# Performance work log

Hardware: AMD Instinct MI355X
Metric: run time of the kernel (lower is better)

## Reference

```python
import jax, jax.numpy as jnp
import numpy as np

EMBED_DIM = 2048
NUM_HEADS = 32
NUM_KV_HEADS = 8
HEAD_DIM = EMBED_DIM // NUM_HEADS  # 64
KV_DIM = HEAD_DIM * NUM_KV_HEADS   # 512
Q_PER_KV = NUM_HEADS // NUM_KV_HEADS  # 4


def setup_inputs() -> dict:
    key = jax.random.key(0)
    ks = jax.random.split(key, 9)
    s = 1.0 / np.sqrt(EMBED_DIM)
    x = jax.random.normal(ks[0], (2, 2048, EMBED_DIM), dtype=jnp.float32)
    Wq = jax.random.uniform(ks[1], (EMBED_DIM, EMBED_DIM), jnp.float32, -s, s)
    bq = jax.random.uniform(ks[2], (EMBED_DIM,), jnp.float32, -s, s)
    Wk = jax.random.uniform(ks[3], (KV_DIM, EMBED_DIM), jnp.float32, -s, s)
    bk = jax.random.uniform(ks[4], (KV_DIM,), jnp.float32, -s, s)
    Wv = jax.random.uniform(ks[5], (KV_DIM, EMBED_DIM), jnp.float32, -s, s)
    bv = jax.random.uniform(ks[6], (KV_DIM,), jnp.float32, -s, s)
    Wo = jax.random.uniform(ks[7], (EMBED_DIM, EMBED_DIM), jnp.float32, -s, s)
    bo = jax.random.uniform(ks[8], (EMBED_DIM,), jnp.float32, -s, s)
    return {"x": x, "Wq": Wq, "bq": bq, "Wk": Wk, "bk": bk,
            "Wv": Wv, "bv": bv, "Wo": Wo, "bo": bo}


def reference(x, Wq, bq, Wk, bk, Wv, bv, Wo, bo):
    B, S, E = x.shape
    # projections (torch Linear: x @ W.T + b)
    q = x @ Wq.T + bq                       # [B,S,E]
    k = x @ Wk.T + bk                       # [B,S,KV_DIM]
    v = x @ Wv.T + bv
    # [B, num_kv, q_per_kv, S, D] and [B, num_kv, S, D] -- GQA grouping
    # avoids repeat_interleave duplication while computing identical math
    q = q.reshape(B, S, NUM_KV_HEADS, Q_PER_KV, HEAD_DIM).transpose(0, 2, 3, 1, 4)
    k = k.reshape(B, S, NUM_KV_HEADS, HEAD_DIM).transpose(0, 2, 1, 3)
    v = v.reshape(B, S, NUM_KV_HEADS, HEAD_DIM).transpose(0, 2, 1, 3)
    scale = 1.0 / np.sqrt(HEAD_DIM).astype(np.float32)
    scores = jnp.einsum('bgqsd,bgtd->bgqst', q, k) * scale  # [B,G,Qpk,S,S]
    causal = jnp.triu(jnp.ones((S, S), dtype=bool), k=1)
    scores = jnp.where(causal, jnp.float32(-jnp.inf), scores)
    attn = jax.nn.softmax(scores, axis=-1)
    out = jnp.einsum('bgqst,bgtd->bgqsd', attn, v)          # [B,G,Qpk,S,D]
    # back to [B,S,E]: head order matches repeat_interleave (kv-major)
    out = out.transpose(0, 3, 1, 2, 4).reshape(B, S, E)
    return out @ Wo.T + bo
```

## Files before the change

kernel.cpp:

```cpp
#include <hip/hip_runtime.h>
#include <stdint.h>

#define EMBED  2048
#define SEQ    2048
#define BATCH  2
#define NHEADS 32
#define NKV    8
#define HDIM   64
#define KVD    512
#define MTOT   (BATCH*SEQ)
#define QKVN   (EMBED + 2*KVD)

typedef __bf16 bf16x8 __attribute__((ext_vector_type(8)));
typedef float  f32x4  __attribute__((ext_vector_type(4)));
typedef float  f32x8v __attribute__((ext_vector_type(8)));
typedef float  f32x2v __attribute__((ext_vector_type(2)));
typedef float  f32x16 __attribute__((ext_vector_type(16)));

#define QSCALE 0.18033688f
#define M2     11.541560f

static __device__ __forceinline__ unsigned short f2bf(float f) {
    union { float f; unsigned int u; } v; v.f = f;
    return (unsigned short)((v.u + 0x7fffu + ((v.u >> 16) & 1u)) >> 16);
}

static __device__ __forceinline__ void gload_lds16(const void* g, void* l) {
    __builtin_amdgcn_global_load_lds(
        (const __attribute__((address_space(1))) void*)g,
        (__attribute__((address_space(3))) void*)l, 16, 0, 0);
}

template<int N> static __device__ __forceinline__ void waitvm() {
    if constexpr (N == 2) asm volatile("s_waitcnt vmcnt(2)" ::: "memory");
    else if constexpr (N == 3) asm volatile("s_waitcnt vmcnt(3)" ::: "memory");
    else if constexpr (N == 5) asm volatile("s_waitcnt vmcnt(5)" ::: "memory");
    else asm volatile("s_waitcnt vmcnt(4)" ::: "memory");
}

static __device__ __forceinline__ void cast4(const float* __restrict__ in,
                                             unsigned short* __restrict__ out, int i) {
    float4 f = reinterpret_cast<const float4*>(in)[i];
    ushort4 o;
    o.x = f2bf(f.x); o.y = f2bf(f.y); o.z = f2bf(f.z); o.w = f2bf(f.w);
    reinterpret_cast<ushort4*>(out)[i] = o;
}

__global__ __launch_bounds__(256)
void prep(const float* __restrict__ x,  const float* __restrict__ Wq,
          const float* __restrict__ Wk, const float* __restrict__ Wv,
          const float* __restrict__ Wo, const float* __restrict__ bq,
          const float* __restrict__ bk, const float* __restrict__ bv,
          unsigned short* __restrict__ xb, unsigned short* __restrict__ Wqkvb,
          unsigned short* __restrict__ Wob, float* __restrict__ bqkv)
{
    const int t0 = blockIdx.x * blockDim.x + threadIdx.x;
    const int st = gridDim.x * blockDim.x;
    for (int i = t0; i < (MTOT * EMBED) / 4;  i += st) cast4(x,  xb, i);
    for (int i = t0; i < (EMBED * EMBED) / 4; i += st) cast4(Wq, Wqkvb, i);
    for (int i = t0; i < (KVD * EMBED) / 4;   i += st) cast4(Wk, Wqkvb + EMBED * EMBED, i);
    for (int i = t0; i < (KVD * EMBED) / 4;   i += st) cast4(Wv, Wqkvb + (EMBED + KVD) * EMBED, i);
    for (int i = t0; i < (EMBED * EMBED) / 4; i += st) cast4(Wo, Wob, i);
    if (t0 < QKVN / 4) {
        float4 v = (t0 < EMBED / 4) ? reinterpret_cast<const float4*>(bq)[t0]
                 : (t0 < (EMBED + KVD) / 4) ? reinterpret_cast<const float4*>(bk)[t0 - EMBED / 4]
                 : reinterpret_cast<const float4*>(bv)[t0 - (EMBED + KVD) / 4];
        reinterpret_cast<float4*>(bqkv)[t0] = v;
    }
}

__global__ __launch_bounds__(256)
void transpose_v(const unsigned short* __restrict__ qkv,
                 unsigned short* __restrict__ vt)
{
    __shared__ __align__(16) unsigned short T[64][72];
    const int bg = blockIdx.x & 15;
    const int bt = blockIdx.x >> 4;
    const int b  = bg >> 3, g = bg & 7;
    const int tid = threadIdx.x;
    const int tr  = tid >> 2, c = tid & 3;

    const unsigned short* src = qkv + ((size_t)(b * SEQ + bt * 64 + tr)) * QKVN
                              + (EMBED + KVD) + g * HDIM + c * 16;
    uint4 v0 = *reinterpret_cast<const uint4*>(src);
    uint4 v1 = *reinterpret_cast<const uint4*>(src + 8);
    *reinterpret_cast<uint4*>(&T[tr][c * 16])     = v0;
    *reinterpret_cast<uint4*>(&T[tr][c * 16 + 8]) = v1;
    __syncthreads();

    const int dr = tr;
    unsigned short o[16];
#pragma unroll
    for (int j = 0; j < 16; ++j) o[j] = T[c * 16 + j][dr];
    unsigned short* dst = vt + ((size_t)(bg * 64 + dr)) * SEQ + bt * 64 + c * 16;
    *reinterpret_cast<uint4*>(dst)     = *reinterpret_cast<uint4*>(o);
    *reinterpret_cast<uint4*>(dst + 8) = *reinterpret_cast<uint4*>(o + 8);
}

__global__ __launch_bounds__(512, 1)
void gemm192(const unsigned short* __restrict__ A,
             const unsigned short* __restrict__ B,
             const float* __restrict__ bias,
             unsigned short* __restrict__ C, int M, int N, int K)
{
    constexpr int ASZ   = 256 * 128;
    constexpr int BSZ   = 192 * 128;
    constexpr int AHALF = ASZ / 2;
    constexpr int BUFSZ = ASZ + BSZ;

    __shared__ __align__(16) char lds[2 * BUFSZ];

    const int tid = threadIdx.x;
    const int l   = tid & 63;
    const int w   = tid >> 6;
    const int wr  = w >> 2, wc = w & 3;
    const int lr15 = l & 15;
    const int lkb  = (l >> 4) * 16;

    const int nwg = gridDim.x;
    const int cpx = nwg >> 3;
    const int bid = blockIdx.x;
    const int swz = (bid & 7) * cpx + (bid >> 3);
    const int NMB = M / 256;
    const int m0  = (swz % NMB) * 256;
    const int n0  = (swz / NMB) * 192;

    unsigned offA[2][2], dA[2][2];
#pragma unroll
    for (int q = 0; q < 2; ++q)
#pragma unroll
        for (int j = 0; j < 2; ++j) {
            int L  = q * AHALF + (tid + j * 512) * 16;
            int R  = L >> 7;
            int cb = (L & 127) ^ ((R & 7) << 4);
            int lrow = ((R >> 6) & 1) * 128 + (R >> 7) * 64 + (R & 63);
            offA[q][j] = (unsigned)((m0 + lrow) * K * 2 + cb);
            dA[q][j]   = (unsigned)L;
        }
    unsigned offB[3], dB[3];
#pragma unroll
    for (int q = 0; q < 3; ++q) {
        int L  = q * 8192 + tid * 16;
        int R  = L >> 7;
        int cb = (L & 127) ^ ((R & 7) << 4);
        offB[q] = (unsigned)((n0 + R) * K * 2 + cb);
        dB[q]   = (unsigned)(ASZ + L);
    }

#define STAGE_A(q, bw, ku) { _Pragma("unroll") \
    for (int j_ = 0; j_ < 2; ++j_) \
        gload_lds16((const char*)A + offA[q][j_] + (unsigned)(ku) * 128u, (bw) + dA[q][j_]); }
#define STAGE_B(q, bw, ku) \
    gload_lds16((const char*)B + offB[q] + (unsigned)(ku) * 128u, (bw) + dB[q]);

    auto rdA = [&](const char* br, int mi, int kk) -> bf16x8 {
        int row  = (mi >> 2) * 128 + wr * 64 + (mi & 3) * 16 + lr15;
        int byte = (row * 128 + kk * 64 + lkb) ^ ((row & 7) << 4);
        return *reinterpret_cast<const bf16x8*>(br + byte);
    };
    auto rdB = [&](const char* br, int ni, int kk) -> bf16x8 {
        int row  = ni * 64 + wc * 16 + lr15;
        int byte = (row * 128 + kk * 64 + lkb) ^ ((row & 7) << 4);
        return *reinterpret_cast<const bf16x8*>(br + ASZ + byte);
    };

    f32x4 acc[8][3] = {};
    bf16x8 afrLo[4][2], afrHi[4][2], bf[3][2];

    STAGE_A(0, lds, 0); STAGE_B(0, lds, 0); STAGE_B(1, lds, 0);
    STAGE_B(2, lds, 0); STAGE_A(1, lds, 0);
    waitvm<3>();
    __builtin_amdgcn_s_barrier();
#pragma unroll
    for (int mi = 0; mi < 4; ++mi)
#pragma unroll
        for (int kk = 0; kk < 2; ++kk) afrLo[mi][kk] = rdA(lds, mi, kk);
#pragma unroll
    for (int kk = 0; kk < 2; ++kk) bf[0][kk] = rdB(lds, 0, kk);

    const int NKT = K >> 6;
    for (int u = 0; u < NKT; ++u) {
        char* br = lds + (u & 1) * BUFSZ;
        char* bw = lds + ((u & 1) ^ 1) * BUFSZ;
        const bool pf = (u + 1 < NKT);
        const int  ku = u + 1;

        if (pf) STAGE_A(0, bw, ku);
#pragma unroll
        for (int kk = 0; kk < 2; ++kk) bf[1][kk] = rdB(br, 1, kk);
        __builtin_amdgcn_s_setprio(1);
#pragma unroll
        for (int mi = 0; mi < 4; ++mi)
#pragma unroll
            for (int kk = 0; kk < 2; ++kk)
                acc[mi][0] = __builtin_amdgcn_mfma_f32_16x16x32_bf16(afrLo[mi][kk], bf[0][kk], acc[mi][0], 0, 0, 0);
        __builtin_amdgcn_s_setprio(0);
        waitvm<4>();
        __builtin_amdgcn_s_barrier();

        if (pf) STAGE_B(0, bw, ku);
#pragma unroll
        for (int kk = 0; kk < 2; ++kk) bf[2][kk] = rdB(br, 2, kk);
        __builtin_amdgcn_s_setprio(1);
#pragma unroll
        for (int mi = 0; mi < 4; ++mi)
#pragma unroll
            for (int kk = 0; kk < 2; ++kk)
                acc[mi][1] = __builtin_amdgcn_mfma_f32_16x16x32_bf16(afrLo[mi][kk], bf[1][kk], acc[mi][1], 0, 0, 0);
        __builtin_amdgcn_s_setprio(0);
        waitvm<3>();
        __builtin_amdgcn_s_barrier();

        if (pf) STAGE_B(1, bw, ku);
#pragma unroll
        for (int mi = 0; mi < 4; ++mi)
#pragma unroll
            for (int kk = 0; kk < 2; ++kk) afrHi[mi][kk] = rdA(br, 4 + mi, kk);
        __builtin_amdgcn_s_setprio(1);
#pragma unroll
        for (int mi = 0; mi < 4; ++mi)
#pragma unroll
            for (int kk = 0; kk < 2; ++kk)
                acc[mi][2] = __builtin_amdgcn_mfma_f32_16x16x32_bf16(afrLo[mi][kk], bf[2][kk], acc[mi][2], 0, 0, 0);
        __builtin_amdgcn_s_setprio(0);

        if (pf) STAGE_B(2, bw, ku);
        __builtin_amdgcn_s_setprio(1);
#pragma unroll
        for (int mi = 0; mi < 4; ++mi)
#pragma unroll
            for (int kk = 0; kk < 2; ++kk)
                acc[4 + mi][0] = __builtin_amdgcn_mfma_f32_16x16x32_bf16(afrHi[mi][kk], bf[0][kk], acc[4 + mi][0], 0, 0, 0);
        __builtin_amdgcn_s_setprio(0);

        if (pf) STAGE_A(1, bw, ku);
        __builtin_amdgcn_s_setprio(1);
#pragma unroll
        for (int mi = 0; mi < 4; ++mi)
#pragma unroll
            for (int kk = 0; kk < 2; ++kk)
                acc[4 + mi][1] = __builtin_amdgcn_mfma_f32_16x16x32_bf16(afrHi[mi][kk], bf[1][kk], acc[4 + mi][1], 0, 0, 0);
        __builtin_amdgcn_s_setprio(0);

        __builtin_amdgcn_s_setprio(1);
#pragma unroll
        for (int mi = 0; mi < 4; ++mi)
#pragma unroll
            for (int kk = 0; kk < 2; ++kk)
                acc[4 + mi][2] = __builtin_amdgcn_mfma_f32_16x16x32_bf16(afrHi[mi][kk], bf[2][kk], acc[4 + mi][2], 0, 0, 0);
        __builtin_amdgcn_s_setprio(0);
        waitvm<3>();
        __builtin_amdgcn_s_barrier();
        if (pf) {
#pragma unroll
            for (int mi = 0; mi < 4; ++mi)
#pragma unroll
                for (int kk = 0; kk < 2; ++kk) afrLo[mi][kk] = rdA(bw, mi, kk);
#pragma unroll
            for (int kk = 0; kk < 2; ++kk) bf[0][kk] = rdB(bw, 0, kk);
        }
    }
#undef STAGE_A
#undef STAGE_B

    float bv[3];
#pragma unroll
    for (int ni = 0; ni < 3; ++ni) bv[ni] = bias[n0 + ni * 64 + wc * 16 + lr15];
#pragma unroll
    for (int mi = 0; mi < 8; ++mi)
#pragma unroll
        for (int ni = 0; ni < 3; ++ni)
#pragma unroll
            for (int r = 0; r < 4; ++r) {
                int row = m0 + wr * 128 + mi * 16 + (l >> 4) * 4 + r;
                int col = n0 + ni * 64 + wc * 16 + lr15;
                C[(size_t)row * N + col] = f2bf(acc[mi][ni][r] + bv[ni]);
            }
}

template<int WM, bool OUT_BF16>
__global__ __launch_bounds__(512, 1)
void gemm8p(const unsigned short* __restrict__ A,
            const unsigned short* __restrict__ B,
            const float* __restrict__ bias,
            void* __restrict__ C, int M, int N, int K)
{
    constexpr int BM    = WM * 32;
    constexpr int ASZ   = BM * 128;
    constexpr int BSZ   = 256 * 128;
    constexpr int AHALF = ASZ / 2;
    constexpr int AL    = AHALF / 8192;
    constexpr int BUFSZ = ASZ + BSZ;

    __shared__ __align__(16) char lds[2 * BUFSZ];

    const int tid = threadIdx.x;
    const int l   = tid & 63;
    const int w   = tid >> 6;
    const int wr  = w >> 2, wc = w & 3;
    const int lr15 = l & 15;
    const int lkb  = (l >> 4) * 16;

    const int nwg = gridDim.x;
    const int cpx = nwg >> 3;
    const int bid = blockIdx.x;
    const int swz = (bid & 7) * cpx + (bid >> 3);
    const int NMB = M / BM;
    const int m0  = (swz % NMB) * BM;
    const int n0  = (swz / NMB) * 256;

    unsigned offA[2][AL], dA[2][AL];
#pragma unroll
    for (int q = 0; q < 2; ++q)
#pragma unroll
        for (int j = 0; j < AL; ++j) {
            int L  = q * AHALF + (tid + j * 512) * 16;
            int R  = L >> 7;
            int cb = (L & 127) ^ ((R & 7) << 4);
            int lrow;
            if constexpr (WM == 8) lrow = ((R >> 6) & 1) * 128 + (R >> 7) * 64 + (R & 63);
            else                   lrow = ((R >> 5) & 1) * 64  + (R >> 6) * 32 + (R & 31);
            offA[q][j] = (unsigned)((m0 + lrow) * K * 2 + cb);
            dA[q][j]   = (unsigned)L;
        }
    unsigned offB[2][2], dB[2][2];
#pragma unroll
    for (int q = 0; q < 2; ++q)
#pragma unroll
        for (int j = 0; j < 2; ++j) {
            int L  = q * 16384 + (tid + j * 512) * 16;
            int R  = L >> 7;
            int cb = (L & 127) ^ ((R & 7) << 4);
            int lrow = ((R >> 5) & 3) * 64 + (R >> 7) * 32 + (R & 31);
            offB[q][j] = (unsigned)((n0 + lrow) * K * 2 + cb);
            dB[q][j]   = (unsigned)(ASZ + L);
        }

#define STAGE_A(q, bw, ku) { _Pragma("unroll") \
    for (int j_ = 0; j_ < AL; ++j_) \
        gload_lds16((const char*)A + offA[q][j_] + (unsigned)(ku) * 128u, (bw) + dA[q][j_]); }
#define STAGE_B(q, bw, ku) { _Pragma("unroll") \
    for (int j_ = 0; j_ < 2; ++j_) \
        gload_lds16((const char*)B + offB[q][j_] + (unsigned)(ku) * 128u, (bw) + dB[q][j_]); }

    auto rdA = [&](const char* br, int mi, int kk) -> bf16x8 {
        int row;
        if constexpr (WM == 8) row = (mi >> 2) * 128 + wr * 64 + (mi & 3) * 16 + lr15;
        else                   row = (mi >> 1) * 64  + wr * 32 + (mi & 1) * 16 + lr15;
        int byte = (row * 128 + kk * 64 + lkb) ^ ((row & 7) << 4);
        return *reinterpret_cast<const bf16x8*>(br + byte);
    };
    auto rdB = [&](const char* br, int ni, int kk) -> bf16x8 {
        int row  = (ni >> 1) * 128 + wc * 32 + (ni & 1) * 16 + lr15;
        int byte = (row * 128 + kk * 64 + lkb) ^ ((row & 7) << 4);
        return *reinterpret_cast<const bf16x8*>(br + ASZ + byte);
    };

    f32x4 acc[WM][4] = {};
    bf16x8 afr[WM / 2][2], bf0[2][2], bf1[2][2];

    STAGE_A(0, lds, 0); STAGE_B(0, lds, 0); STAGE_B(1, lds, 0); STAGE_A(1, lds, 0);
    waitvm<2 + AL>();
    __builtin_amdgcn_s_barrier();

    const int NKT = K >> 6;
    for (int u = 0; u < NKT; ++u) {
        char* br = lds + (u & 1) * BUFSZ;
        char* bw = lds + ((u & 1) ^ 1) * BUFSZ;
        const bool pf = (u + 1 < NKT);
        const int  ku = u + 1;

        if (pf) STAGE_A(0, bw, ku);
#pragma unroll
        for (int mi = 0; mi < WM / 2; ++mi)
#pragma unroll
            for (int kk = 0; kk < 2; ++kk) afr[mi][kk] = rdA(br, mi, kk);
#pragma unroll
        for (int ni = 0; ni < 2; ++ni)
#pragma unroll
            for (int kk = 0; kk < 2; ++kk) bf0[ni][kk] = rdB(br, ni, kk);
        __builtin_amdgcn_s_setprio(1);
#pragma unroll
        for (int mi = 0; mi < WM / 2; ++mi)
#pragma unroll
            for (int ni = 0; ni < 2; ++ni)
#pragma unroll
                for (int kk = 0; kk < 2; ++kk)
                    acc[mi][ni] = __builtin_amdgcn_mfma_f32_16x16x32_bf16(afr[mi][kk], bf0[ni][kk], acc[mi][ni], 0, 0, 0);
        __builtin_amdgcn_s_setprio(0);
        waitvm<2 * AL>();
        __builtin_amdgcn_s_barrier();

        if (pf) STAGE_B(0, bw, ku);
#pragma unroll
        for (int ni = 0; ni < 2; ++ni)
#pragma unroll
            for (int kk = 0; kk < 2; ++kk) bf1[ni][kk] = rdB(br, 2 + ni, kk);
        __builtin_amdgcn_s_setprio(1);
#pragma unroll
        for (int mi = 0; mi < WM / 2; ++mi)
#pragma unroll
            for (int ni = 0; ni < 2; ++ni)
#pragma unroll
                for (int kk = 0; kk < 2; ++kk)
                    acc[mi][2 + ni] = __builtin_amdgcn_mfma_f32_16x16x32_bf16(afr[mi][kk], bf1[ni][kk], acc[mi][2 + ni], 0, 0, 0);
        __builtin_amdgcn_s_setprio(0);
        waitvm<AL + 2>();
        __builtin_amdgcn_s_barrier();

        if (pf) STAGE_B(1, bw, ku);
#pragma unroll
        for (int mi = 0; mi < WM / 2; ++mi)
#pragma unroll
            for (int kk = 0; kk < 2; ++kk) afr[mi][kk] = rdA(br, WM / 2 + mi, kk);
        __builtin_amdgcn_s_setprio(1);
#pragma unroll
        for (int mi = 0; mi < WM / 2; ++mi)
#pragma unroll
            for (int ni = 0; ni < 2; ++ni)
#pragma unroll
                for (int kk = 0; kk < 2; ++kk)
                    acc[WM / 2 + mi][ni] = __builtin_amdgcn_mfma_f32_16x16x32_bf16(afr[mi][kk], bf0[ni][kk], acc[WM / 2 + mi][ni], 0, 0, 0);
        __builtin_amdgcn_s_setprio(0);

        if (pf) STAGE_A(1, bw, ku);
        __builtin_amdgcn_s_setprio(1);
#pragma unroll
        for (int mi = 0; mi < WM / 2; ++mi)
#pragma unroll
            for (int ni = 0; ni < 2; ++ni)
#pragma unroll
                for (int kk = 0; kk < 2; ++kk)
                    acc[WM / 2 + mi][2 + ni] = __builtin_amdgcn_mfma_f32_16x16x32_bf16(afr[mi][kk], bf1[ni][kk], acc[WM / 2 + mi][2 + ni], 0, 0, 0);
        __builtin_amdgcn_s_setprio(0);
        waitvm<2 + AL>();
        __builtin_amdgcn_s_barrier();
    }
#undef STAGE_A
#undef STAGE_B

    float bv[4];
#pragma unroll
    for (int ni = 0; ni < 4; ++ni) bv[ni] = bias[n0 + wc * 64 + ni * 16 + lr15];
#pragma unroll
    for (int mi = 0; mi < WM; ++mi)
#pragma unroll
        for (int ni = 0; ni < 4; ++ni)
#pragma unroll
            for (int r = 0; r < 4; ++r) {
                int row = m0 + wr * (WM * 16) + mi * 16 + (l >> 4) * 4 + r;
                int col = n0 + wc * 64 + ni * 16 + lr15;
                float v = acc[mi][ni][r] + bv[ni];
                if constexpr (OUT_BF16)
                    ((unsigned short*)C)[(size_t)row * N + col] = f2bf(v);
                else
                    ((float*)C)[(size_t)row * N + col] = v;
            }
}

static __device__ __forceinline__ bf16x8 pack_frag(float p0, float p1, float p2, float p3,
                                                   float p4, float p5, float p6, float p7) {
    unsigned int w0, w1, w2, w3;
    asm("v_cvt_pk_bf16_f32 %0, %1, %2" : "=v"(w0) : "v"(p0), "v"(p1));
    asm("v_cvt_pk_bf16_f32 %0, %1, %2" : "=v"(w1) : "v"(p2), "v"(p3));
    asm("v_cvt_pk_bf16_f32 %0, %1, %2" : "=v"(w2) : "v"(p4), "v"(p5));
    asm("v_cvt_pk_bf16_f32 %0, %1, %2" : "=v"(w3) : "v"(p6), "v"(p7));
    asm("v_permlane32_swap_b32 %0, %1" : "+v"(w0), "+v"(w2));
    asm("v_permlane32_swap_b32 %0, %1" : "+v"(w1), "+v"(w3));
    union { unsigned int u[4]; bf16x8 v; } uu;
    uu.u[0] = w0; uu.u[1] = w1; uu.u[2] = w2; uu.u[3] = w3;
    return uu.v;
}

static __device__ __forceinline__ float hsum32(f32x16 a, f32x16 b) {
    f32x16 t = a + b;
    f32x8v u = __builtin_shufflevector(t, t, 0,1,2,3,4,5,6,7)
             + __builtin_shufflevector(t, t, 8,9,10,11,12,13,14,15);
    f32x4 v4 = __builtin_shufflevector(u, u, 0,1,2,3)
             + __builtin_shufflevector(u, u, 4,5,6,7);
    f32x2v v2 = __builtin_shufflevector(v4, v4, 0,1)
              + __builtin_shufflevector(v4, v4, 2,3);
    return v2[0] + v2[1];
}

__global__ __launch_bounds__(256, 2)
void gqa_attn(const unsigned short* __restrict__ qkv,
              const unsigned short* __restrict__ vtg,
              unsigned short* __restrict__ ctx)
{
    __shared__ __align__(16) unsigned short Ks[2][64 * 64];
    __shared__ __align__(16) unsigned short Vs[2][64 * 64];

    const int bid = blockIdx.x;
    const int g   = bid & 7;
    const int bh  = (bid >> 3) & 3;
    const int b   = bh >> 1;
    const int hp  = bh & 1;
    const int idx = bid >> 5;
    const int s   = idx >> 3, i = idx & 7;
    const int qt  = (s == 0) ? 31 - i : (s == 1) ? i : (s == 2) ? 23 - i : 8 + i;
    const int NT  = qt + 1;

    const int tid = threadIdx.x;
    const int l   = tid & 63;
    const int w   = tid >> 6;
    const int hi  = l >> 5;
    const int lq  = l & 31;

    const int h   = g * 4 + hp * 2 + (w >> 1);
    const int q0  = qt * 64 + (w & 1) * 32;
    const size_t rowb = (size_t)b * SEQ;
    const int kbase = EMBED + g * HDIM;

    bf16x8 qf[4];
    {
        const char* qa = (const char*)qkv + ((rowb + q0 + lq) * QKVN + (size_t)h * HDIM) * 2;
#pragma unroll
        for (int ks = 0; ks < 4; ++ks) {
            bf16x8 ta = *reinterpret_cast<const bf16x8*>(qa + (ks * 16 + hi * 8) * 2);
#pragma unroll
            for (int j = 0; j < 8; ++j)
                ta[j] = (__bf16)((float)ta[j] * QSCALE);
            qf[ks] = ta;
        }
    }

    f32x16 acc0 = {}, acc1 = {};
    float l_run = 0.0f;

    const int Lk0 = tid << 4;
    const int Lk1 = (tid + 256) << 4;
    const int Tk0 = Lk0 ^ (((Lk0 >> 7) & 7) << 4);
    const int Tk1 = Lk1 ^ (((Lk1 >> 7) & 7) << 4);
    const int kr0 = Tk0 >> 7, ko0 = Tk0 & 127;
    const int kr1 = Tk1 >> 7, ko1 = Tk1 & 127;

    const char* vtb = (const char*)vtg + (size_t)(b * 8 + g) * HDIM * SEQ * 2;

#define STAGE_KV(buf, tt) { \
    gload_lds16((const char*)qkv + ((rowb + (tt) + kr0) * QKVN + kbase) * 2 + ko0, (char*)Ks[buf] + Lk0); \
    gload_lds16((const char*)qkv + ((rowb + (tt) + kr1) * QKVN + kbase) * 2 + ko1, (char*)Ks[buf] + Lk1); \
    gload_lds16(vtb + ((size_t)kr0 * SEQ + (tt)) * 2 + ko0, (char*)Vs[buf] + Lk0); \
    gload_lds16(vtb + ((size_t)kr1 * SEQ + (tt)) * 2 + ko1, (char*)Vs[buf] + Lk1); }

    STAGE_KV(0, 0);
    __syncthreads();

    for (int kt = 0; kt < NT; ++kt) {
        const int cur = kt & 1;
        const int t0  = kt * 64;
        const bool haveNext = (kt + 1 < NT);
        if (haveNext) STAGE_KV(cur ^ 1, t0 + 64);

        const char* KsBuf = (const char*)Ks[cur];
        f32x16 s0 = {}, s1 = {};
        __builtin_amdgcn_s_setprio(1);
#pragma unroll
        for (int ks = 0; ks < 4; ++ks) {
            const int colb = (ks * 16 + hi * 8) * 2;
            int a0 = (lq * 128 + colb) ^ ((lq & 7) << 4);
            bf16x8 kf0 = *reinterpret_cast<const bf16x8*>(KsBuf + a0);
            s0 = __builtin_amdgcn_mfma_f32_32x32x16_bf16(kf0, qf[ks], s0, 0, 0, 0);
            int r1 = 32 + lq;
            int a1 = (r1 * 128 + colb) ^ ((r1 & 7) << 4);
            bf16x8 kf1 = *reinterpret_cast<const bf16x8*>(KsBuf + a1);
            s1 = __builtin_amdgcn_mfma_f32_32x32x16_bf16(kf1, qf[ks], s1, 0, 0, 0);
        }
        __builtin_amdgcn_s_setprio(0);

        if (kt == qt) {
            const int q = q0 + lq;
#pragma unroll
            for (int r = 0; r < 16; ++r) {
                int tg = t0 + (r & 3) + 8 * (r >> 2) + 4 * hi;
                if (tg > q) s0[r] = -1e30f;
                if (tg + 32 > q) s1[r] = -1e30f;
            }
        }

        s0 = s0 - M2;
        s1 = s1 - M2;
#pragma unroll
        for (int r = 0; r < 16; ++r) {
            s0[r] = __builtin_amdgcn_exp2f(s0[r]);
            s1[r] = __builtin_amdgcn_exp2f(s1[r]);
        }

        float rs = hsum32(s0, s1);
        l_run += rs + __shfl_xor(rs, 32);

        bf16x8 pa[4];
        pa[0] = pack_frag(s0[0], s0[1], s0[2], s0[3], s0[4], s0[5], s0[6], s0[7]);
        pa[1] = pack_frag(s0[8], s0[9], s0[10], s0[11], s0[12], s0[13], s0[14], s0[15]);
        pa[2] = pack_frag(s1[0], s1[1], s1[2], s1[3], s1[4], s1[5], s1[6], s1[7]);
        pa[3] = pack_frag(s1[8], s1[9], s1[10], s1[11], s1[12], s1[13], s1[14], s1[15]);

        const char* VsBuf = (const char*)Vs[cur];
        __builtin_amdgcn_s_setprio(1);
#pragma unroll
        for (int ks = 0; ks < 4; ++ks) {
            const int colb = (ks * 16 + hi * 8) * 2;
            int a0 = (lq * 128 + colb) ^ ((lq & 7) << 4);
            bf16x8 vf0 = *reinterpret_cast<const bf16x8*>(VsBuf + a0);
            acc0 = __builtin_amdgcn_mfma_f32_32x32x16_bf16(pa[ks], vf0, acc0, 0, 0, 0);
            int d1 = 32 + lq;
            int a1 = (d1 * 128 + colb) ^ ((d1 & 7) << 4);
            bf16x8 vf1 = *reinterpret_cast<const bf16x8*>(VsBuf + a1);
            acc1 = __builtin_amdgcn_mfma_f32_32x32x16_bf16(pa[ks], vf1, acc1, 0, 0, 0);
        }
        __builtin_amdgcn_s_setprio(0);

        if (haveNext) __syncthreads();
    }
#undef STAGE_KV

#pragma unroll
    for (int r = 0; r < 16; ++r) {
        int qr  = (r & 3) + 8 * (r >> 2) + 4 * hi;
        int col = h * HDIM + lq;
        float lr = __shfl(l_run, qr);
        size_t row = rowb + q0 + qr;
        ctx[row * EMBED + col]      = f2bf(acc0[r] / lr);
        ctx[row * EMBED + col + 32] = f2bf(acc1[r] / lr);
    }
}

extern "C" void kernel_launch(void* const* d_in, const int* in_sizes, int n_in,
                              void* d_out, int out_size, void* d_ws, size_t ws_size,
                              hipStream_t stream) {
    (void)in_sizes; (void)n_in; (void)out_size; (void)ws_size;
    const float* x  = (const float*)d_in[0];
    const float* Wq = (const float*)d_in[1];
    const float* bq = (const float*)d_in[2];
    const float* Wk = (const float*)d_in[3];
    const float* bk = (const float*)d_in[4];
    const float* Wv = (const float*)d_in[5];
    const float* bv = (const float*)d_in[6];
    const float* Wo = (const float*)d_in[7];
    const float* bo = (const float*)d_in[8];
    float* out = (float*)d_out;

    char* ws = (char*)d_ws;
    unsigned short* xb    = (unsigned short*)(ws);
    unsigned short* Wqkvb = (unsigned short*)(ws + 16777216);
    unsigned short* Wob   = (unsigned short*)(ws + 29360128);
    float*          bqkv  = (float*)         (ws + 37748736);
    unsigned short* QKVb  = (unsigned short*)(ws + 37761024);
    unsigned short* ctx   = (unsigned short*)(ws + 62926848);
    unsigned short* VT    = xb;

    prep<<<2048, 256, 0, stream>>>(x, Wq, Wk, Wv, Wo, bq, bk, bv,
                                   xb, Wqkvb, Wob, bqkv);

    gemm192<<<dim3(256), 512, 0, stream>>>(
        xb, Wqkvb, bqkv, QKVb, MTOT, QKVN, EMBED);

    transpose_v<<<dim3(512), 256, 0, stream>>>(QKVb, VT);

    gqa_attn<<<dim3(1024), 256, 0, stream>>>(QKVb, VT, ctx);

    gemm8p<4, false><<<dim3(256), 512, 0, stream>>>(
        ctx, Wob, bo, out, MTOT, EMBED, EMBED);
}
```

Before: 157.9 us.

## Reshape output projection GEMM to 256x128 tiles with prefetched LDS fragments

Replaces the templated output-projection GEMM, which used 128x256 tiles, with a dedicated kernel using 256x128 tiles (M by N). Each wave now covers 128 rows by 32 columns. The first A and B fragments for the next K-step are read from LDS at the end of the current iteration, so LDS reads overlap the barrier and MFMA work. The wait counts are retuned for the new load mix. This changes per-wave register use and the A/B reuse ratio, and the hand-set vmcnt values must match the load order exactly.

```diff
diff --git a/kernel.cpp b/kernel.cpp
--- a/kernel.cpp
+++ b/kernel.cpp
@@ -32,7 +32,8 @@
 }
 
 template<int N> static __device__ __forceinline__ void waitvm() {
-    if constexpr (N == 2) asm volatile("s_waitcnt vmcnt(2)" ::: "memory");
+    if constexpr (N == 0) asm volatile("s_waitcnt vmcnt(0)" ::: "memory");
+    else if constexpr (N == 2) asm volatile("s_waitcnt vmcnt(2)" ::: "memory");
     else if constexpr (N == 3) asm volatile("s_waitcnt vmcnt(3)" ::: "memory");
     else if constexpr (N == 5) asm volatile("s_waitcnt vmcnt(5)" ::: "memory");
     else asm volatile("s_waitcnt vmcnt(4)" ::: "memory");
@@ -278,18 +279,15 @@
             }
 }
 
-template<int WM, bool OUT_BF16>
 __global__ __launch_bounds__(512, 1)
-void gemm8p(const unsigned short* __restrict__ A,
-            const unsigned short* __restrict__ B,
-            const float* __restrict__ bias,
-            void* __restrict__ C, int M, int N, int K)
+void gemmO(const unsigned short* __restrict__ A,
+           const unsigned short* __restrict__ B,
+           const float* __restrict__ bias,
+           float* __restrict__ C, int M, int N, int K)
 {
-    constexpr int BM    = WM * 32;
-    constexpr int ASZ   = BM * 128;
-    constexpr int BSZ   = 256 * 128;
+    constexpr int ASZ   = 256 * 128;
+    constexpr int BSZ   = 128 * 128;
     constexpr int AHALF = ASZ / 2;
-    constexpr int AL    = AHALF / 8192;
     constexpr int BUFSZ = ASZ + BSZ;
 
     __shared__ __align__(16) char lds[2 * BUFSZ];
@@ -305,63 +303,63 @@
     const int cpx = nwg >> 3;
     const int bid = blockIdx.x;
     const int swz = (bid & 7) * cpx + (bid >> 3);
-    const int NMB = M / BM;
-    const int m0  = (swz % NMB) * BM;
-    const int n0  = (swz / NMB) * 256;
-
-    unsigned offA[2][AL], dA[2][AL];
+    const int NMB = M / 256;
+    const int m0  = (swz % NMB) * 256;
+    const int n0  = (swz / NMB) * 128;
+
+    unsigned offA[2][2], dA[2][2];
 #pragma unroll
     for (int q = 0; q < 2; ++q)
 #pragma unroll
-        for (int j = 0; j < AL; ++j) {
+        for (int j = 0; j < 2; ++j) {
             int L  = q * AHALF + (tid + j * 512) * 16;
             int R  = L >> 7;
             int cb = (L & 127) ^ ((R & 7) << 4);
-            int lrow;
-            if constexpr (WM == 8) lrow = ((R >> 6) & 1) * 128 + (R >> 7) * 64 + (R & 63);
-            else                   lrow = ((R >> 5) & 1) * 64  + (R >> 6) * 32 + (R & 31);
+            int lrow = ((R >> 6) & 1) * 128 + (R >> 7) * 64 + (R & 63);
             offA[q][j] = (unsigned)((m0 + lrow) * K * 2 + cb);
             dA[q][j]   = (unsigned)L;
         }
-    unsigned offB[2][2], dB[2][2];
-#pragma unroll
-    for (int q = 0; q < 2; ++q)
-#pragma unroll
-        for (int j = 0; j < 2; ++j) {
-            int L  = q * 16384 + (tid + j * 512) * 16;
-            int R  = L >> 7;
-            int cb = (L & 127) ^ ((R & 7) << 4);
-            int lrow = ((R >> 5) & 3) * 64 + (R >> 7) * 32 + (R & 31);
-            offB[q][j] = (unsigned)((n0 + lrow) * K * 2 + cb);
-            dB[q][j]   = (unsigned)(ASZ + L);
-        }
+    unsigned offB[2], dB[2];
+#pragma unroll
+    for (int q = 0; q < 2; ++q) {
+        int L  = q * 8192 + tid * 16;
+        int R  = L >> 7;
+        int cb = (L & 127) ^ ((R & 7) << 4);
+        int r6 = R & 63;
+        int lrow = (r6 >> 4) * 32 + q * 16 + (r6 & 15);
+        offB[q] = (unsigned)((n0 + lrow) * K * 2 + cb);
+        dB[q]   = (unsigned)(ASZ + L);
+    }
 
 #define STAGE_A(q, bw, ku) { _Pragma("unroll") \
-    for (int j_ = 0; j_ < AL; ++j_) \
+    for (int j_ = 0; j_ < 2; ++j_) \
         gload_lds16((const char*)A + offA[q][j_] + (unsigned)(ku) * 128u, (bw) + dA[q][j_]); }
-#define STAGE_B(q, bw, ku) { _Pragma("unroll") \
-    for (int j_ = 0; j_ < 2; ++j_) \
-        gload_lds16((const char*)B + offB[q][j_] + (unsigned)(ku) * 128u, (bw) + dB[q][j_]); }
+#define STAGE_B(q, bw, ku) \
+    gload_lds16((const char*)B + offB[q] + (unsigned)(ku) * 128u, (bw) + dB[q]);
 
     auto rdA = [&](const char* br, int mi, int kk) -> bf16x8 {
-        int row;
-        if constexpr (WM == 8) row = (mi >> 2) * 128 + wr * 64 + (mi & 3) * 16 + lr15;
-        else                   row = (mi >> 1) * 64  + wr * 32 + (mi & 1) * 16 + lr15;
+        int row  = (mi >> 2) * 128 + wr * 64 + (mi & 3) * 16 + lr15;
         int byte = (row * 128 + kk * 64 + lkb) ^ ((row & 7) << 4);
         return *reinterpret_cast<const bf16x8*>(br + byte);
     };
     auto rdB = [&](const char* br, int ni, int kk) -> bf16x8 {
-        int row  = (ni >> 1) * 128 + wc * 32 + (ni & 1) * 16 + lr15;
+        int row  = ni * 64 + wc * 16 + lr15;
         int byte = (row * 128 + kk * 64 + lkb) ^ ((row & 7) << 4);
         return *reinterpret_cast<const bf16x8*>(br + ASZ + byte);
     };
 
-    f32x4 acc[WM][4] = {};
-    bf16x8 afr[WM / 2][2], bf0[2][2], bf1[2][2];
+    f32x4 acc[8][2] = {};
+    bf16x8 afrLo[4][2], afrHi[4][2], bf[2][2];
 
     STAGE_A(0, lds, 0); STAGE_B(0, lds, 0); STAGE_B(1, lds, 0); STAGE_A(1, lds, 0);
-    waitvm<2 + AL>();
+    waitvm<3>();
     __builtin_amdgcn_s_barrier();
+#pragma unroll
+    for (int mi = 0; mi < 4; ++mi)
+#pragma unroll
+        for (int kk = 0; kk < 2; ++kk) afrLo[mi][kk] = rdA(lds, mi, kk);
+#pragma unroll
+    for (int kk = 0; kk < 2; ++kk) bf[0][kk] = rdB(lds, 0, kk);
 
     const int NKT = K >> 6;
     for (int u = 0; u < NKT; ++u) {
@@ -371,90 +369,76 @@
         const int  ku = u + 1;
 
         if (pf) STAGE_A(0, bw, ku);
-#pragma unroll
-        for (int mi = 0; mi < WM / 2; ++mi)
-#pragma unroll
-            for (int kk = 0; kk < 2; ++kk) afr[mi][kk] = rdA(br, mi, kk);
-#pragma unroll
-        for (int ni = 0; ni < 2; ++ni)
-#pragma unroll
-            for (int kk = 0; kk < 2; ++kk) bf0[ni][kk] = rdB(br, ni, kk);
-        __builtin_amdgcn_s_setprio(1);
-#pragma unroll
-        for (int mi = 0; mi < WM / 2; ++mi)
-#pragma unroll
-            for (int ni = 0; ni < 2; ++ni)
-#pragma unroll
-                for (int kk = 0; kk < 2; ++kk)
-                    acc[mi][ni] = __builtin_amdgcn_mfma_f32_16x16x32_bf16(afr[mi][kk], bf0[ni][kk], acc[mi][ni], 0, 0, 0);
-        __builtin_amdgcn_s_setprio(0);
-        waitvm<2 * AL>();
+        __builtin_amdgcn_s_setprio(1);
+#pragma unroll
+        for (int mi = 0; mi < 4; ++mi)
+#pragma unroll
+            for (int kk = 0; kk < 2; ++kk)
+                acc[mi][0] = __builtin_amdgcn_mfma_f32_16x16x32_bf16(afrLo[mi][kk], bf[0][kk], acc[mi][0], 0, 0, 0);
+        __builtin_amdgcn_s_setprio(0);
+        if (pf) waitvm<4>(); else waitvm<2>();
         __builtin_amdgcn_s_barrier();
+#pragma unroll
+        for (int kk = 0; kk < 2; ++kk) bf[1][kk] = rdB(br, 1, kk);
 
         if (pf) STAGE_B(0, bw, ku);
-#pragma unroll
-        for (int ni = 0; ni < 2; ++ni)
-#pragma unroll
-            for (int kk = 0; kk < 2; ++kk) bf1[ni][kk] = rdB(br, 2 + ni, kk);
-        __builtin_amdgcn_s_setprio(1);
-#pragma unroll
-        for (int mi = 0; mi < WM / 2; ++mi)
-#pragma unroll
-            for (int ni = 0; ni < 2; ++ni)
-#pragma unroll
-                for (int kk = 0; kk < 2; ++kk)
-                    acc[mi][2 + ni] = __builtin_amdgcn_mfma_f32_16x16x32_bf16(afr[mi][kk], bf1[ni][kk], acc[mi][2 + ni], 0, 0, 0);
-        __builtin_amdgcn_s_setprio(0);
-        waitvm<AL + 2>();
+        __builtin_amdgcn_s_setprio(1);
+#pragma unroll
+        for (int mi = 0; mi < 4; ++mi)
+#pragma unroll
+            for (int kk = 0; kk < 2; ++kk)
+                acc[mi][1] = __builtin_amdgcn_mfma_f32_16x16x32_bf16(afrLo[mi][kk], bf[1][kk], acc[mi][1], 0, 0, 0);
+        __builtin_amdgcn_s_setprio(0);
+        if (pf) waitvm<3>(); else waitvm<0>();
         __builtin_amdgcn_s_barrier();
+#pragma unroll
+        for (int mi = 0; mi < 4; ++mi)
+#pragma unroll
+            for (int kk = 0; kk < 2; ++kk) afrHi[mi][kk] = rdA(br, 4 + mi, kk);
 
         if (pf) STAGE_B(1, bw, ku);
-#pragma unroll
-        for (int mi = 0; mi < WM / 2; ++mi)
-#pragma unroll
-            for (int kk = 0; kk < 2; ++kk) afr[mi][kk] = rdA(br, WM / 2 + mi, kk);
-        __builtin_amdgcn_s_setprio(1);
-#pragma unroll
-        for (int mi = 0; mi < WM / 2; ++mi)
-#pragma unroll
-            for (int ni = 0; ni < 2; ++ni)
-#pragma unroll
-                for (int kk = 0; kk < 2; ++kk)
-                    acc[WM / 2 + mi][ni] = __builtin_amdgcn_mfma_f32_16x16x32_bf16(afr[mi][kk], bf0[ni][kk], acc[WM / 2 + mi][ni], 0, 0, 0);
+        __builtin_amdgcn_s_setprio(1);
+#pragma unroll
+        for (int mi = 0; mi < 4; ++mi)
+#pragma unroll
+            for (int kk = 0; kk < 2; ++kk)
+                acc[4 + mi][0] = __builtin_amdgcn_mfma_f32_16x16x32_bf16(afrHi[mi][kk], bf[0][kk], acc[4 + mi][0], 0, 0, 0);
         __builtin_amdgcn_s_setprio(0);
 
         if (pf) STAGE_A(1, bw, ku);
         __builtin_amdgcn_s_setprio(1);
 #pragma unroll
-        for (int mi = 0; mi < WM / 2; ++mi)
-#pragma unroll
-            for (int ni = 0; ni < 2; ++ni)
-#pragma unroll
-                for (int kk = 0; kk < 2; ++kk)
-                    acc[WM / 2 + mi][2 + ni] = __builtin_amdgcn_mfma_f32_16x16x32_bf16(afr[mi][kk], bf1[ni][kk], acc[WM / 2 + mi][2 + ni], 0, 0, 0);
-        __builtin_amdgcn_s_setprio(0);
-        waitvm<2 + AL>();
-        __builtin_amdgcn_s_barrier();
+        for (int mi = 0; mi < 4; ++mi)
+#pragma unroll
+            for (int kk = 0; kk < 2; ++kk)
+                acc[4 + mi][1] = __builtin_amdgcn_mfma_f32_16x16x32_bf16(afrHi[mi][kk], bf[1][kk], acc[4 + mi][1], 0, 0, 0);
+        __builtin_amdgcn_s_setprio(0);
+        if (pf) {
+            waitvm<3>();
+            __builtin_amdgcn_s_barrier();
+#pragma unroll
+            for (int mi = 0; mi < 4; ++mi)
+#pragma unroll
+                for (int kk = 0; kk < 2; ++kk) afrLo[mi][kk] = rdA(bw, mi, kk);
+#pragma unroll
+            for (int kk = 0; kk < 2; ++kk) bf[0][kk] = rdB(bw, 0, kk);
+        }
     }
 #undef STAGE_A
 #undef STAGE_B
 
-    float bv[4];
-#pragma unroll
-    for (int ni = 0; ni < 4; ++ni) bv[ni] = bias[n0 + wc * 64 + ni * 16 + lr15];
-#pragma unroll
-    for (int mi = 0; mi < WM; ++mi)
-#pragma unroll
-        for (int ni = 0; ni < 4; ++ni)
+    float bv[2];
+#pragma unroll
+    for (int ni = 0; ni < 2; ++ni) bv[ni] = bias[n0 + wc * 32 + ni * 16 + lr15];
+#pragma unroll
+    for (int mi = 0; mi < 8; ++mi)
+#pragma unroll
+        for (int ni = 0; ni < 2; ++ni)
 #pragma unroll
             for (int r = 0; r < 4; ++r) {
-                int row = m0 + wr * (WM * 16) + mi * 16 + (l >> 4) * 4 + r;
-                int col = n0 + wc * 64 + ni * 16 + lr15;
-                float v = acc[mi][ni][r] + bv[ni];
-                if constexpr (OUT_BF16)
-                    ((unsigned short*)C)[(size_t)row * N + col] = f2bf(v);
-                else
-                    ((float*)C)[(size_t)row * N + col] = v;
+                int row = m0 + wr * 128 + mi * 16 + (l >> 4) * 4 + r;
+                int col = n0 + wc * 32 + ni * 16 + lr15;
+                C[(size_t)row * N + col] = acc[mi][ni][r] + bv[ni];
             }
 }
 
@@ -659,6 +643,6 @@
 
     gqa_attn<<<dim3(1024), 256, 0, stream>>>(QKVb, VT, ctx);
 
-    gemm8p<4, false><<<dim3(256), 512, 0, stream>>>(
+    gemmO<<<dim3(256), 512, 0, stream>>>(
         ctx, Wob, bo, out, MTOT, EMBED, EMBED);
 }
```

Measured after the change: 157.7 us, median of 2. No clear change (-0.1%).
